# Optimization experiments

Hardware: AMD Instinct MI355X
Metric: run time of the kernel (lower is better)

The kernel has to match this reference:

```python
import jax, jax.numpy as jnp
import numpy as np

EPS = 1e-20  # safe_normalize epsilon


def setup_inputs() -> dict:
    key = jax.random.key(0)
    k1, k2 = jax.random.split(key)
    B, N = 512, 512
    normals = jax.random.normal(k1, (B, N, 3), dtype=jnp.float32)
    weights = jax.random.uniform(k2, (B, N, 1), dtype=jnp.float32)
    return {"normals": normals, "weights": weights}


def reference(normals, weights):
    # normals: [B, N, 3]; weights: [B, N, 1] (unused by the original math,
    # it is only used for zeros_like shape).
    B, N, _ = normals.shape
    # Pairwise cosine matrix: [B, N, N]
    cos = jnp.clip(jnp.einsum('bid,bjd->bij', normals, normals), -1.0, 1.0)
    offdiag = 1.0 - jnp.eye(N, dtype=normals.dtype)  # exclude i == j
    # mask diagonal before arccos to keep grads clean at cos==1
    cos = jnp.where(offdiag > 0, cos, 0.0)
    w_pair = jnp.exp(-jnp.arccos(cos)) * offdiag  # [B, N, N]
    # each pair (i, j), i != j, contributes its weight to both rows -> row sum
    new_weights = jnp.sum(w_pair, axis=2, keepdims=True)  # [B, N, 1]
    new_weights = new_weights / jnp.max(new_weights)
    n = jnp.sum(new_weights * normals, axis=1)  # [B, 3]
    # safe_normalize
    n = n / jnp.sqrt(jnp.maximum(jnp.sum(n * n, axis=-1, keepdims=True), EPS))
    return n
```

## Files before the change

kernel.cpp:

```cpp
#include <hip/hip_runtime.h>
#include <math.h>

#define BATCH 512
#define NPTS  512

__device__ __forceinline__ float rot1(float v) {
    return __int_as_float(__builtin_amdgcn_update_dpp(
        __float_as_int(v), __float_as_int(v), 0x134, 0xF, 0xF, false));
}

__device__ __forceinline__ float pair_w_exact(float d) {
    d = __builtin_amdgcn_fmed3f(d, -1.f, 1.f);
    float a  = fabsf(d);
    float t  = 1.f - a;
    float sq = __builtin_amdgcn_sqrtf(t);
    float p  = fmaf(-0.00182139f, a, 0.00962291f);
    p = fmaf(p, a, -0.02465296f);
    p = fmaf(p, a,  0.04456757f);
    p = fmaf(p, a, -0.07238623f);
    p = fmaf(p, a,  0.12836958f);
    p = fmaf(p, a, -0.30960063f);
    p = fmaf(p, a,  2.26618007f);
    float q = sq * p;
    float e = (d < 0.f) ? (4.53236014f - q) : q;
    return __builtin_amdgcn_exp2f(-e);
}

__device__ __forceinline__ float pair_w(float d, const float2* __restrict__ wtab) {
    float idx_f = __builtin_amdgcn_fmed3f(fmaf(d, 256.f, 256.f), 0.f, 512.f);
    int   idx   = (int)idx_f;
    idx = min(idx, 511);
    float frac  = idx_f - (float)idx;
    float2 c = wtab[idx];
    return fmaf(frac, c.y, c.x);
}

template<int K0, int K1, bool TAIL>
__device__ __forceinline__ void do_seg(
    const float* __restrict__ sx, const float* __restrict__ sy,
    const float* __restrict__ sz, const float2* __restrict__ wtab,
    int v, int lane, float xi, float yi, float zi,
    float& accA, float* __restrict__ racc)
{
    const int bi = v * 64 + lane;
    float bx = sx[bi], by = sy[bi], bz = sz[bi];
    float bacc = 0.f;
    #pragma unroll
    for (int r = 0; r < K0; ++r) { bx = rot1(bx); by = rot1(by); bz = rot1(bz); }
    #pragma unroll 8
    for (int k = K0; k <= K1; ++k) {
        float d = fmaf(xi, bx, fmaf(yi, by, zi * bz));
        float w = pair_w(d, wtab);
        accA += w;
        bacc += w;
        bx = rot1(bx); by = rot1(by); bz = rot1(bz); bacc = rot1(bacc);
    }
    if (TAIL) {
        float d = fmaf(xi, bx, fmaf(yi, by, zi * bz));
        accA += pair_w(d, wtab);
    }
    const int m = (lane + K1 + 1) & 63;
    atomicAdd(&racc[v * 64 + m], bacc);
}

__global__ __launch_bounds__(NPTS) void normals_fused_kernel(
    const float* __restrict__ normals, float* __restrict__ out)
{
    __shared__ float  sx[NPTS], sy[NPTS], sz[NPTS];
    __shared__ float  racc[NPTS];
    __shared__ float2 wtab[512];
    __shared__ float  rx[8], ry[8], rz[8];
    const int b    = blockIdx.x;
    const int tid  = threadIdx.x;
    const int wave = tid >> 6, lane = tid & 63;
    const float* base = normals + (size_t)b * NPTS * 3;

    {
        float d0 = (float)tid       * (1.f / 256.f) - 1.f;
        float d1 = (float)(tid + 1) * (1.f / 256.f) - 1.f;
        float w0 = pair_w_exact(d0);
        float w1 = pair_w_exact(d1);
        wtab[tid] = make_float2(w0, w1 - w0);
    }
    for (int k = tid; k < NPTS * 3; k += NPTS) {
        float val = base[k];
        int r = k / 3, c = k - r * 3;
        float* dst = (c == 0) ? sx : (c == 1) ? sy : sz;
        dst[r] = val;
    }
    racc[tid] = 0.f;
    __syncthreads();

    const float xi = sx[tid], yi = sy[tid], zi = sz[tid];
    float accA = 0.f;

    do_seg<1, 31, true >(sx, sy, sz, wtab, wave,           lane, xi, yi, zi, accA, racc);
    do_seg<0, 63, false>(sx, sy, sz, wtab, (wave + 1) & 7, lane, xi, yi, zi, accA, racc);
    do_seg<0, 63, false>(sx, sy, sz, wtab, (wave + 2) & 7, lane, xi, yi, zi, accA, racc);
    do_seg<0, 63, false>(sx, sy, sz, wtab, (wave + 3) & 7, lane, xi, yi, zi, accA, racc);
    if (wave < 4) do_seg<0, 31, false>(sx, sy, sz, wtab, wave + 4, lane, xi, yi, zi, accA, racc);
    else          do_seg<1, 32, false>(sx, sy, sz, wtab, wave - 4, lane, xi, yi, zi, accA, racc);

    __syncthreads();
    float s = accA + racc[tid];

    float ax = s * xi, ay = s * yi, az = s * zi;

    for (int off = 32; off > 0; off >>= 1) {
        ax += __shfl_down(ax, off, 64);
        ay += __shfl_down(ay, off, 64);
        az += __shfl_down(az, off, 64);
    }
    if (lane == 0) { rx[wave] = ax; ry[wave] = ay; rz[wave] = az; }
    __syncthreads();

    if (tid == 0) {
        float nx = 0.f, ny = 0.f, nz = 0.f;
        #pragma unroll
        for (int w = 0; w < 8; ++w) { nx += rx[w]; ny += ry[w]; nz += rz[w]; }
        float len2 = fmaf(nx, nx, fmaf(ny, ny, nz * nz));
        float inv  = rsqrtf(fmaxf(len2, 1e-20f));
        out[b * 3 + 0] = nx * inv;
        out[b * 3 + 1] = ny * inv;
        out[b * 3 + 2] = nz * inv;
    }
}

extern "C" void kernel_launch(void* const* d_in, const int* in_sizes, int n_in,
                              void* d_out, int out_size, void* d_ws, size_t ws_size,
                              hipStream_t stream) {
    const float* normals = (const float*)d_in[0];
    float* out = (float*)d_out;
    normals_fused_kernel<<<BATCH, NPTS, 0, stream>>>(normals, out);
}
```

Measured before the change: 87.76 us.

## Split each batch's pair work across two blocks and add a normalize kernel

Each batch is now processed by two blocks that each evaluate about half of the pairwise segments. Each block writes a partial weighted-normal sum to workspace, and a second single-block kernel adds the two halves and normalizes. The aim is more blocks in flight for better occupancy and latency hiding. The cost is a duplicated table build and input load per block plus an extra kernel launch. A sentinel table entry also replaces the index clamp in the lookup.

```diff
diff --git a/kernel.cpp b/kernel.cpp
--- a/kernel.cpp
+++ b/kernel.cpp
@@ -29,7 +29,6 @@
 __device__ __forceinline__ float pair_w(float d, const float2* __restrict__ wtab) {
     float idx_f = __builtin_amdgcn_fmed3f(fmaf(d, 256.f, 256.f), 0.f, 512.f);
     int   idx   = (int)idx_f;
-    idx = min(idx, 511);
     float frac  = idx_f - (float)idx;
     float2 c = wtab[idx];
     return fmaf(frac, c.y, c.x);
@@ -63,24 +62,25 @@
     atomicAdd(&racc[v * 64 + m], bacc);
 }
 
-__global__ __launch_bounds__(NPTS) void normals_fused_kernel(
-    const float* __restrict__ normals, float* __restrict__ out)
+__global__ __launch_bounds__(512, 8) void pairs_kernel(
+    const float* __restrict__ normals, float* __restrict__ ws)
 {
     __shared__ float  sx[NPTS], sy[NPTS], sz[NPTS];
     __shared__ float  racc[NPTS];
-    __shared__ float2 wtab[512];
+    __shared__ float2 wtab[513];
     __shared__ float  rx[8], ry[8], rz[8];
-    const int b    = blockIdx.x;
-    const int tid  = threadIdx.x;
-    const int wave = tid >> 6, lane = tid & 63;
+    const int bx_id = blockIdx.x;
+    const int b     = bx_id >> 1, half = bx_id & 1;
+    const int tid   = threadIdx.x;
+    const int wave  = tid >> 6, lane = tid & 63;
     const float* base = normals + (size_t)b * NPTS * 3;
 
     {
-        float d0 = (float)tid       * (1.f / 256.f) - 1.f;
-        float d1 = (float)(tid + 1) * (1.f / 256.f) - 1.f;
+        float d0 = (float)tid * (1.f / 256.f) - 1.f;
         float w0 = pair_w_exact(d0);
-        float w1 = pair_w_exact(d1);
+        float w1 = pair_w_exact(d0 + (1.f / 256.f));
         wtab[tid] = make_float2(w0, w1 - w0);
+        if (tid == 0) wtab[512] = make_float2(1.f, 0.f);
     }
     for (int k = tid; k < NPTS * 3; k += NPTS) {
         float val = base[k];
@@ -94,12 +94,15 @@
     const float xi = sx[tid], yi = sy[tid], zi = sz[tid];
     float accA = 0.f;
 
-    do_seg<1, 31, true >(sx, sy, sz, wtab, wave,           lane, xi, yi, zi, accA, racc);
-    do_seg<0, 63, false>(sx, sy, sz, wtab, (wave + 1) & 7, lane, xi, yi, zi, accA, racc);
-    do_seg<0, 63, false>(sx, sy, sz, wtab, (wave + 2) & 7, lane, xi, yi, zi, accA, racc);
-    do_seg<0, 63, false>(sx, sy, sz, wtab, (wave + 3) & 7, lane, xi, yi, zi, accA, racc);
-    if (wave < 4) do_seg<0, 31, false>(sx, sy, sz, wtab, wave + 4, lane, xi, yi, zi, accA, racc);
-    else          do_seg<1, 32, false>(sx, sy, sz, wtab, wave - 4, lane, xi, yi, zi, accA, racc);
+    if (half == 0) {
+        do_seg<1, 31, true >(sx, sy, sz, wtab, wave,           lane, xi, yi, zi, accA, racc);
+        do_seg<0, 63, false>(sx, sy, sz, wtab, (wave + 1) & 7, lane, xi, yi, zi, accA, racc);
+        if (wave < 4) do_seg<0, 31, false>(sx, sy, sz, wtab, wave + 4, lane, xi, yi, zi, accA, racc);
+        else          do_seg<1, 32, false>(sx, sy, sz, wtab, wave - 4, lane, xi, yi, zi, accA, racc);
+    } else {
+        do_seg<0, 63, false>(sx, sy, sz, wtab, (wave + 2) & 7, lane, xi, yi, zi, accA, racc);
+        do_seg<0, 63, false>(sx, sy, sz, wtab, (wave + 3) & 7, lane, xi, yi, zi, accA, racc);
+    }
 
     __syncthreads();
     float s = accA + racc[tid];
@@ -118,12 +121,22 @@
         float nx = 0.f, ny = 0.f, nz = 0.f;
         #pragma unroll
         for (int w = 0; w < 8; ++w) { nx += rx[w]; ny += ry[w]; nz += rz[w]; }
-        float len2 = fmaf(nx, nx, fmaf(ny, ny, nz * nz));
-        float inv  = rsqrtf(fmaxf(len2, 1e-20f));
-        out[b * 3 + 0] = nx * inv;
-        out[b * 3 + 1] = ny * inv;
-        out[b * 3 + 2] = nz * inv;
+        ((float4*)ws)[bx_id] = make_float4(nx, ny, nz, 0.f);
     }
+}
+
+__global__ __launch_bounds__(512) void norm_kernel(
+    const float* __restrict__ ws, float* __restrict__ out)
+{
+    const int t = threadIdx.x;
+    float4 p0 = ((const float4*)ws)[2 * t];
+    float4 p1 = ((const float4*)ws)[2 * t + 1];
+    float nx = p0.x + p1.x, ny = p0.y + p1.y, nz = p0.z + p1.z;
+    float len2 = fmaf(nx, nx, fmaf(ny, ny, nz * nz));
+    float inv  = rsqrtf(fmaxf(len2, 1e-20f));
+    out[t * 3 + 0] = nx * inv;
+    out[t * 3 + 1] = ny * inv;
+    out[t * 3 + 2] = nz * inv;
 }
 
 extern "C" void kernel_launch(void* const* d_in, const int* in_sizes, int n_in,
@@ -131,5 +144,7 @@
                               hipStream_t stream) {
     const float* normals = (const float*)d_in[0];
     float* out = (float*)d_out;
-    normals_fused_kernel<<<BATCH, NPTS, 0, stream>>>(normals, out);
+    float* ws  = (float*)d_ws;
+    pairs_kernel<<<2 * BATCH, NPTS, 0, stream>>>(normals, ws);
+    norm_kernel<<<1, BATCH, 0, stream>>>(ws, out);
 }
```

Result: no change. 86.14 us (-1.9%).
